# Performance work log

Hardware: AMD Instinct MI355X
Metric: run time of the kernel (lower is better)

Reference implementation:

```python
import jax, jax.numpy as jnp
import numpy as np

N_NODES = 50000
N_EDGES = 800000
IN_DIM, HIDDEN, Z_DIM = 32, 64, 32


def gcn_conv(x, W, b, src, dst, n):
    """PyG-style GCNConv: h = D^{-1/2}(A+I)D^{-1/2} (x W) + b."""
    h = x @ W  # [N, out]
    loop = jnp.arange(n, dtype=src.dtype)
    s = jnp.concatenate([src, loop])  # add self-loops
    d = jnp.concatenate([dst, loop])
    deg = jax.ops.segment_sum(jnp.ones(s.shape, h.dtype), d, num_segments=n)
    dinv = jax.lax.rsqrt(jnp.maximum(deg, jnp.asarray(1.0, h.dtype)))
    norm = dinv[s] * dinv[d]                       # [E+N]
    msg = h[s] * norm[:, None]                     # gather + scale
    out = jax.ops.segment_sum(msg, d, num_segments=n)  # scatter-add
    return out + b


def setup_inputs() -> dict:
    key = jax.random.key(0)
    ks = jax.random.split(key, 8)
    sc = lambda fan_in: 1.0 / np.sqrt(fan_in)
    x = jax.random.normal(ks[0], (N_NODES, IN_DIM), jnp.float32)
    edge_index = jax.random.randint(ks[1], (2, N_EDGES), 0, N_NODES, jnp.int64)
    W1 = jax.random.normal(ks[2], (IN_DIM, HIDDEN), jnp.float32) * sc(IN_DIM)
    b1 = jnp.zeros((HIDDEN,), jnp.float32)
    W2 = jax.random.normal(ks[3], (HIDDEN, HIDDEN), jnp.float32) * sc(HIDDEN)
    b2 = jnp.zeros((HIDDEN,), jnp.float32)
    W_mu = jax.random.normal(ks[4], (HIDDEN, Z_DIM), jnp.float32) * sc(HIDDEN)
    b_mu = jnp.zeros((Z_DIM,), jnp.float32)
    W_lv = jax.random.normal(ks[5], (HIDDEN, Z_DIM), jnp.float32) * sc(HIDDEN)
    b_lv = jnp.zeros((Z_DIM,), jnp.float32)
    eps = jax.random.normal(ks[6], (N_NODES, Z_DIM), jnp.float32)
    return {"x": x, "edge_index": edge_index, "W1": W1, "b1": b1, "W2": W2,
            "b2": b2, "W_mu": W_mu, "b_mu": b_mu, "W_lv": W_lv, "b_lv": b_lv,
            "eps": eps}


def reference(x, edge_index, W1, b1, W2, b2, W_mu, b_mu, W_lv, b_lv, eps):
    src, dst = edge_index[0], edge_index[1]
    n = x.shape[0]
    h = jax.nn.relu(gcn_conv(x, W1, b1, src, dst, n))
    h = jax.nn.relu(gcn_conv(h, W2, b2, src, dst, n))
    # dropout p=0.0 -> identity
    mu = gcn_conv(h, W_mu, b_mu, src, dst, n)
    logvar = gcn_conv(h, W_lv, b_lv, src, dst, n)
    z = mu + jnp.exp(0.5 * logvar) * eps  # reparametrize
    return (z, mu, logvar)
```

## Files before the change

### kernel.cpp

```cpp
#include <hip/hip_runtime.h>
#include <math.h>

#define N_NODES 50000
#define N_EDGES 800000
#define IN_DIM 32
#define HIDDEN 64
#define Z_DIM 32
#define SCAN_B 256
#define NB_SCAN ((N_NODES + SCAN_B - 1) / SCAN_B)
#define N_XCD 8
#define NPX ((N_NODES + N_XCD - 1) / N_XCD)
#define SLICE 2048
#define N_SLICE ((N_EDGES + SLICE - 1) / SLICE)
#define SCAT_B (N_SLICE * N_XCD)
#define FB 1024
#define CPAD 16

__device__ __forceinline__ unsigned short f2bf(float f) {
    unsigned int u = __float_as_uint(f);
    u += 0x7fffu + ((u >> 16) & 1u);
    return (unsigned short)(u >> 16);
}

__device__ __forceinline__ int detect64(const int* raw) {
    int lane = threadIdx.x & 63;
    int odd = raw[2 * lane + 1];
    unsigned long long b = __ballot(odd != 0);
    return (b == 0ULL) ? 1 : 0;
}

__device__ __forceinline__ void fma8(float w, uint4 f, float acc[8]) {
    acc[0] = fmaf(w, __uint_as_float(f.x << 16),         acc[0]);
    acc[1] = fmaf(w, __uint_as_float(f.x & 0xffff0000u), acc[1]);
    acc[2] = fmaf(w, __uint_as_float(f.y << 16),         acc[2]);
    acc[3] = fmaf(w, __uint_as_float(f.y & 0xffff0000u), acc[3]);
    acc[4] = fmaf(w, __uint_as_float(f.z << 16),         acc[4]);
    acc[5] = fmaf(w, __uint_as_float(f.z & 0xffff0000u), acc[5]);
    acc[6] = fmaf(w, __uint_as_float(f.w << 16),         acc[6]);
    acc[7] = fmaf(w, __uint_as_float(f.w & 0xffff0000u), acc[7]);
}
__device__ __forceinline__ void mul8(float w, uint4 f, float acc[8]) {
    acc[0] = w * __uint_as_float(f.x << 16);
    acc[1] = w * __uint_as_float(f.x & 0xffff0000u);
    acc[2] = w * __uint_as_float(f.y << 16);
    acc[3] = w * __uint_as_float(f.y & 0xffff0000u);
    acc[4] = w * __uint_as_float(f.z << 16);
    acc[5] = w * __uint_as_float(f.z & 0xffff0000u);
    acc[6] = w * __uint_as_float(f.w << 16);
    acc[7] = w * __uint_as_float(f.w & 0xffff0000u);
}

__global__ void prep_a_kernel(const float* __restrict__ x, unsigned short* __restrict__ xb,
                              const void* __restrict__ raw, ushort2* __restrict__ ep0,
                              int* __restrict__ cnt) {
    int is64 = detect64((const int*)raw);
    int i = blockIdx.x * 256 + threadIdx.x;
    if (i < N_NODES * IN_DIM) xb[i] = f2bf(x[i]);
    if (i < N_NODES * CPAD) cnt[i] = 0;
    if (i < N_EDGES) {
        int s, d;
        if (is64) {
            s = (int)((const long long*)raw)[i];
            d = (int)((const long long*)raw)[N_EDGES + i];
        } else {
            s = ((const int*)raw)[i];
            d = ((const int*)raw)[N_EDGES + i];
        }
        ep0[i] = make_ushort2((unsigned short)s, (unsigned short)d);
    }
}

__global__ __launch_bounds__(256) void hist_kernel(const ushort2* __restrict__ ep0,
                                                   int* __restrict__ cnt,
                                                   unsigned short* __restrict__ rank) {
    int xcd = blockIdx.x % N_XCD;
    int sl  = blockIdx.x / N_XCD;
    int lo  = xcd * NPX, hi = lo + NPX;
    int base = sl * SLICE;
#pragma unroll
    for (int j = 0; j < SLICE / 256; j++) {
        int e = base + j * 256 + threadIdx.x;
        if (e < N_EDGES) {
            int d = ep0[e].y;
            if (d >= lo && d < hi)
                rank[e] = (unsigned short)atomicAdd(&cnt[(size_t)d * CPAD], 1);
        }
    }
}

__global__ void scan1_kernel(const int* __restrict__ cnt, int* __restrict__ pre,
                             int* __restrict__ bsum, float* __restrict__ dinv) {
    __shared__ int s[SCAN_B];
    int t = threadIdx.x;
    int g = blockIdx.x * SCAN_B + t;
    int v = (g < N_NODES) ? cnt[(size_t)g * CPAD] : 0;
    if (g < N_NODES) dinv[g] = rsqrtf((float)(v + 1));
    s[t] = v;
    __syncthreads();
    for (int o = 1; o < SCAN_B; o <<= 1) {
        int add = (t >= o) ? s[t - o] : 0;
        __syncthreads();
        s[t] += add;
        __syncthreads();
    }
    if (g < N_NODES) pre[g] = s[t] - v;
    if (t == SCAN_B - 1) bsum[blockIdx.x] = s[t];
}

#define BSUM_SCAN_PROLOGUE(bsum, sb, sx)                                    \
    {                                                                       \
        int t_ = threadIdx.x;                                               \
        int bv_ = (t_ < NB_SCAN) ? bsum[t_] : 0;                            \
        sb[t_] = bv_;                                                       \
        __syncthreads();                                                    \
        for (int o_ = 1; o_ < 256; o_ <<= 1) {                              \
            int a_ = (t_ >= o_) ? sb[t_ - o_] : 0;                          \
            __syncthreads();                                                \
            sb[t_] += a_;                                                   \
            __syncthreads();                                                \
        }                                                                   \
        sx[t_] = sb[t_] - bv_;                                              \
        __syncthreads();                                                    \
    }

__global__ __launch_bounds__(256) void scatter_kernel(
        const ushort2* __restrict__ ep0, const unsigned short* __restrict__ rank,
        const int* __restrict__ pre, const int* __restrict__ bsum,
        const float* __restrict__ dinv, int2* __restrict__ ep) {
    __shared__ int sb[256];
    __shared__ int sx[256];
    BSUM_SCAN_PROLOGUE(bsum, sb, sx)
    int base = blockIdx.x * SLICE;
#pragma unroll
    for (int j = 0; j < SLICE / 256; j++) {
        int e = base + j * 256 + threadIdx.x;
        if (e < N_EDGES) {
            ushort2 sd = ep0[e];
            int d = sd.y;
            int p = pre[d] + sx[d >> 8] + (int)rank[e];
            int s = sd.x;
            ep[p] = make_int2(s, __float_as_int(dinv[s]));
        }
    }
}

__device__ __forceinline__ void agg64(int e0, int e1, int2 pr,
                                      const int2* __restrict__ ep,
                                      const uint4* __restrict__ g4,
                                      int2* eb, int lane, int gsel, int c,
                                      float acc[8]) {
    for (int b0 = e0; b0 < e1; b0 += 64) {
        int cnt = e1 - b0; cnt = cnt > 64 ? 64 : cnt;
        eb[lane] = pr;
        for (int j = 0; j < cnt; j += 16) {
            int2 ew0 = eb[j + gsel];
            int2 ew1 = eb[j + 8 + gsel];
            uint4 f0 = g4[(size_t)ew0.x * 8 + c];
            uint4 f1 = g4[(size_t)ew1.x * 8 + c];
            fma8(__int_as_float(ew0.y), f0, acc);
            fma8(__int_as_float(ew1.y), f1, acc);
        }
        if (b0 + 64 < e1) {
            pr = make_int2(0, 0);
            int idx = b0 + 64 + lane;
            if (idx < e1) pr = ep[idx];
        }
    }
}

__device__ __forceinline__ void agg32(int e0, int e1, int2 pr,
                                      const int2* __restrict__ ep,
                                      const uint4* __restrict__ x4,
                                      int2* eb, int lane, int gsel, int c,
                                      float acc[8]) {
    for (int b0 = e0; b0 < e1; b0 += 64) {
        int cnt = e1 - b0; cnt = cnt > 64 ? 64 : cnt;
        eb[lane] = pr;
        for (int j = 0; j < cnt; j += 32) {
            int2 ew0 = eb[j + gsel];
            int2 ew1 = eb[j + 16 + gsel];
            uint4 f0 = x4[(size_t)ew0.x * 4 + c];
            uint4 f1 = x4[(size_t)ew1.x * 4 + c];
            fma8(__int_as_float(ew0.y), f0, acc);
            fma8(__int_as_float(ew1.y), f1, acc);
        }
        if (b0 + 64 < e1) {
            pr = make_int2(0, 0);
            int idx = b0 + 64 + lane;
            if (idx < e1) pr = ep[idx];
        }
    }
}

__global__ __launch_bounds__(256) void fused_layer32_kernel(
        const int* __restrict__ pre, const int* __restrict__ bsum,
        const int2* __restrict__ ep, const float* __restrict__ dinv,
        const unsigned short* __restrict__ xb,
        const float* __restrict__ W1, const float* __restrict__ b1,
        unsigned short* __restrict__ out) {
    __shared__ int sb[256];
    __shared__ int sx[256];
    __shared__ int2 ebuf[4][64];
    __shared__ float sq[4][32];
    BSUM_SCAN_PROLOGUE(bsum, sb, sx)
    int lane = threadIdx.x & 63;
    int wav  = threadIdx.x >> 6;
    int gsel = lane >> 2;
    int c    = lane & 3;
    const uint4* x4 = (const uint4*)xb;
    int2* eb = &ebuf[wav][0];
    float wcol[IN_DIM];
#pragma unroll
    for (int k = 0; k < IN_DIM; k++) wcol[k] = W1[k * 64 + lane];
    float bb = b1[lane];
    int wid = __builtin_amdgcn_readfirstlane((int)((blockIdx.x * blockDim.x + threadIdx.x) >> 6));
    int nw  = (gridDim.x * blockDim.x) >> 6;
    int v = wid;
    if (v >= N_NODES) return;
    int e0 = pre[v] + sx[v >> 8];
    int e1 = (v + 1 < N_NODES) ? pre[v + 1] + sx[(v + 1) >> 8] : N_EDGES;
    float dv = dinv[v];
    uint4 hv = x4[(size_t)v * 4 + c];
    int2 pr = make_int2(0, 0);
    if (lane < e1 - e0) pr = ep[e0 + lane];
    while (v < N_NODES) {
        int vn = v + nw;
        int e0n = 0, e1n = 0;
        float dvn = 0.0f;
        uint4 hvn = make_uint4(0, 0, 0, 0);
        int2 prn = make_int2(0, 0);
        if (vn < N_NODES) {
            e0n = pre[vn] + sx[vn >> 8];
            e1n = (vn + 1 < N_NODES) ? pre[vn + 1] + sx[(vn + 1) >> 8] : N_EDGES;
            dvn = dinv[vn];
            hvn = x4[(size_t)vn * 4 + c];
            if (lane < e1n - e0n) prn = ep[e0n + lane];
        }
        float sv = (gsel == 0) ? dv : 0.0f;
        float acc[8];
        mul8(sv, hv, acc);
        agg32(e0, e1, pr, ep, x4, eb, lane, gsel, c, acc);
#pragma unroll
        for (int i = 0; i < 8; i++) {
            acc[i] += __shfl_xor(acc[i], 4);
            acc[i] += __shfl_xor(acc[i], 8);
            acc[i] += __shfl_xor(acc[i], 16);
            acc[i] += __shfl_xor(acc[i], 32);
        }
        if (lane < 4) {
            float4* qd = (float4*)(&sq[wav][lane * 8]);
            qd[0] = make_float4(dv * acc[0], dv * acc[1], dv * acc[2], dv * acc[3]);
            qd[1] = make_float4(dv * acc[4], dv * acc[5], dv * acc[6], dv * acc[7]);
        }
        float o0 = bb, o1 = 0.0f, o2 = 0.0f, o3 = 0.0f;
        const float4* q4 = (const float4*)(&sq[wav][0]);
#pragma unroll
        for (int k = 0; k < IN_DIM / 4; k++) {
            float4 tq = q4[k];
            o0 = fmaf(tq.x, wcol[4 * k + 0], o0);
            o1 = fmaf(tq.y, wcol[4 * k + 1], o1);
            o2 = fmaf(tq.z, wcol[4 * k + 2], o2);
            o3 = fmaf(tq.w, wcol[4 * k + 3], o3);
        }
        float o = (o0 + o1) + (o2 + o3);
        out[(size_t)v * 64 + lane] = f2bf(fmaxf(o, 0.0f));
        v = vn; e0 = e0n; e1 = e1n; dv = dvn; hv = hvn; pr = prn;
    }
}

__global__ __launch_bounds__(256) void fused_layer64_kernel(
        const int* __restrict__ pre, const int* __restrict__ bsum,
        const int2* __restrict__ ep, const float* __restrict__ dinv,
        const unsigned short* __restrict__ g,
        const float* __restrict__ W, const float* __restrict__ bias,
        unsigned short* __restrict__ out) {
    __shared__ int sb[256];
    __shared__ int sx[256];
    __shared__ int2 ebuf[4][64];
    __shared__ float sq[4][64];
    BSUM_SCAN_PROLOGUE(bsum, sb, sx)
    int lane = threadIdx.x & 63;
    int wav  = threadIdx.x >> 6;
    int gsel = lane >> 3;
    int c    = lane & 7;
    const uint4* g4 = (const uint4*)g;
    int2* eb = &ebuf[wav][0];
    float wcol[HIDDEN];
#pragma unroll
    for (int k = 0; k < HIDDEN; k++) wcol[k] = W[k * 64 + lane];
    float bb = bias[lane];
    int wid = __builtin_amdgcn_readfirstlane((int)((blockIdx.x * blockDim.x + threadIdx.x) >> 6));
    int nw  = (gridDim.x * blockDim.x) >> 6;
    int v = wid;
    if (v >= N_NODES) return;
    int e0 = pre[v] + sx[v >> 8];
    int e1 = (v + 1 < N_NODES) ? pre[v + 1] + sx[(v + 1) >> 8] : N_EDGES;
    float dv = dinv[v];
    uint4 hv = g4[(size_t)v * 8 + c];
    int2 pr = make_int2(0, 0);
    if (lane < e1 - e0) pr = ep[e0 + lane];
    while (v < N_NODES) {
        int vn = v + nw;
        int e0n = 0, e1n = 0;
        float dvn = 0.0f;
        uint4 hvn = make_uint4(0, 0, 0, 0);
        int2 prn = make_int2(0, 0);
        if (vn < N_NODES) {
            e0n = pre[vn] + sx[vn >> 8];
            e1n = (vn + 1 < N_NODES) ? pre[vn + 1] + sx[(vn + 1) >> 8] : N_EDGES;
            dvn = dinv[vn];
            hvn = g4[(size_t)vn * 8 + c];
            if (lane < e1n - e0n) prn = ep[e0n + lane];
        }
        float sv = (gsel == 0) ? dv : 0.0f;
        float acc[8];
        mul8(sv, hv, acc);
        agg64(e0, e1, pr, ep, g4, eb, lane, gsel, c, acc);
#pragma unroll
        for (int i = 0; i < 8; i++) {
            acc[i] += __shfl_xor(acc[i], 8);
            acc[i] += __shfl_xor(acc[i], 16);
            acc[i] += __shfl_xor(acc[i], 32);
        }
        if (lane < 8) {
            float4* qd = (float4*)(&sq[wav][lane * 8]);
            qd[0] = make_float4(dv * acc[0], dv * acc[1], dv * acc[2], dv * acc[3]);
            qd[1] = make_float4(dv * acc[4], dv * acc[5], dv * acc[6], dv * acc[7]);
        }
        float o0 = bb, o1 = 0.0f, o2 = 0.0f, o3 = 0.0f;
        const float4* q4 = (const float4*)(&sq[wav][0]);
#pragma unroll
        for (int k = 0; k < HIDDEN / 4; k++) {
            float4 tq = q4[k];
            o0 = fmaf(tq.x, wcol[4 * k + 0], o0);
            o1 = fmaf(tq.y, wcol[4 * k + 1], o1);
            o2 = fmaf(tq.z, wcol[4 * k + 2], o2);
            o3 = fmaf(tq.w, wcol[4 * k + 3], o3);
        }
        float o = (o0 + o1) + (o2 + o3);
        out[(size_t)v * 64 + lane] = f2bf(fmaxf(o, 0.0f));
        v = vn; e0 = e0n; e1 = e1n; dv = dvn; hv = hvn; pr = prn;
    }
}

__global__ __launch_bounds__(256) void fused_head_kernel(
        const int* __restrict__ pre, const int* __restrict__ bsum,
        const int2* __restrict__ ep, const float* __restrict__ dinv,
        const unsigned short* __restrict__ g,
        const float* __restrict__ Wmu, const float* __restrict__ Wlv,
        const float* __restrict__ bmu, const float* __restrict__ blv,
        const float* __restrict__ eps, float* __restrict__ outz) {
    __shared__ int sb[256];
    __shared__ int sx[256];
    __shared__ int2 ebuf[4][64];
    __shared__ float sq[4][64];
    BSUM_SCAN_PROLOGUE(bsum, sb, sx)
    int lane = threadIdx.x & 63;
    int wav  = threadIdx.x >> 6;
    int gsel = lane >> 3;
    int c    = lane & 7;
    int f = lane & 31;
    bool hi = lane >= 32;
    const uint4* g4 = (const uint4*)g;
    int2* eb = &ebuf[wav][0];
    float wcol[HIDDEN];
#pragma unroll
    for (int k = 0; k < HIDDEN; k++)
        wcol[k] = hi ? Wlv[k * 32 + f] : Wmu[k * 32 + f];
    float bb = hi ? blv[f] : bmu[f];
    float* z  = outz;
    float* mu = outz + (size_t)N_NODES * Z_DIM;
    float* lv = outz + 2 * (size_t)N_NODES * Z_DIM;
    int wid = __builtin_amdgcn_readfirstlane((int)((blockIdx.x * blockDim.x + threadIdx.x) >> 6));
    int nw  = (gridDim.x * blockDim.x) >> 6;
    int v = wid;
    if (v >= N_NODES) return;
    int e0 = pre[v] + sx[v >> 8];
    int e1 = (v + 1 < N_NODES) ? pre[v + 1] + sx[(v + 1) >> 8] : N_EDGES;
    float dv = dinv[v];
    uint4 hv = g4[(size_t)v * 8 + c];
    int2 pr = make_int2(0, 0);
    if (lane < e1 - e0) pr = ep[e0 + lane];
    while (v < N_NODES) {
        int vn = v + nw;
        int e0n = 0, e1n = 0;
        float dvn = 0.0f;
        uint4 hvn = make_uint4(0, 0, 0, 0);
        int2 prn = make_int2(0, 0);
        if (vn < N_NODES) {
            e0n = pre[vn] + sx[vn >> 8];
            e1n = (vn + 1 < N_NODES) ? pre[vn + 1] + sx[(vn + 1) >> 8] : N_EDGES;
            dvn = dinv[vn];
            hvn = g4[(size_t)vn * 8 + c];
            if (lane < e1n - e0n) prn = ep[e0n + lane];
        }
        float sv = (gsel == 0) ? dv : 0.0f;
        float acc[8];
        mul8(sv, hv, acc);
        agg64(e0, e1, pr, ep, g4, eb, lane, gsel, c, acc);
#pragma unroll
        for (int i = 0; i < 8; i++) {
            acc[i] += __shfl_xor(acc[i], 8);
            acc[i] += __shfl_xor(acc[i], 16);
            acc[i] += __shfl_xor(acc[i], 32);
        }
        if (lane < 8) {
            float4* qd = (float4*)(&sq[wav][lane * 8]);
            qd[0] = make_float4(dv * acc[0], dv * acc[1], dv * acc[2], dv * acc[3]);
            qd[1] = make_float4(dv * acc[4], dv * acc[5], dv * acc[6], dv * acc[7]);
        }
        float m0 = bb, m1 = 0.0f, m2 = 0.0f, m3 = 0.0f;
        const float4* q4 = (const float4*)(&sq[wav][0]);
#pragma unroll
        for (int k = 0; k < HIDDEN / 4; k++) {
            float4 tq = q4[k];
            m0 = fmaf(tq.x, wcol[4 * k + 0], m0);
            m1 = fmaf(tq.y, wcol[4 * k + 1], m1);
            m2 = fmaf(tq.z, wcol[4 * k + 2], m2);
            m3 = fmaf(tq.w, wcol[4 * k + 3], m3);
        }
        float m = (m0 + m1) + (m2 + m3);
        float ev = eps[(size_t)v * Z_DIM + f];
        float t  = expf(0.5f * m) * ev;
        float tlo = __shfl(t, lane | 32);
        size_t o = (size_t)v * Z_DIM + f;
        if (!hi) { mu[o] = m; z[o] = m + tlo; }
        else     { lv[o] = m; }
        v = vn; e0 = e0n; e1 = e1n; dv = dvn; hv = hvn; pr = prn;
    }
}

extern "C" void kernel_launch(void* const* d_in, const int* in_sizes, int n_in,
                              void* d_out, int out_size, void* d_ws, size_t ws_size,
                              hipStream_t stream) {
    const float* x   = (const float*)d_in[0];
    const void*  ei  = d_in[1];
    const float* W1  = (const float*)d_in[2];
    const float* b1  = (const float*)d_in[3];
    const float* W2  = (const float*)d_in[4];
    const float* b2  = (const float*)d_in[5];
    const float* Wmu = (const float*)d_in[6];
    const float* bmu = (const float*)d_in[7];
    const float* Wlv = (const float*)d_in[8];
    const float* blv = (const float*)d_in[9];
    const float* eps = (const float*)d_in[10];
    float* out = (float*)d_out;
    (void)in_sizes; (void)n_in; (void)out_size; (void)ws_size;

    char* ws = (char*)d_ws;
    size_t off = 0;
    auto alloc = [&](size_t bytes) -> void* {
        void* p = ws + off;
        off += (bytes + 255) & ~(size_t)255;
        return p;
    };
    int2*           ep     = (int2*)alloc(sizeof(int2) * N_EDGES);
    ushort2*        ep0    = (ushort2*)alloc(sizeof(ushort2) * N_EDGES);
    unsigned short* rank   = (unsigned short*)alloc(sizeof(short) * N_EDGES);
    int*            pre    = (int*)alloc(sizeof(int) * (N_NODES + 1));
    int*            cnt    = (int*)alloc(sizeof(int) * (size_t)N_NODES * CPAD);
    float*          dinv   = (float*)alloc(sizeof(float) * N_NODES);
    int*            bsum   = (int*)alloc(sizeof(int) * 256);
    unsigned short* xb     = (unsigned short*)alloc(sizeof(short) * (size_t)N_NODES * IN_DIM);
    unsigned short* G      = (unsigned short*)alloc(sizeof(short) * (size_t)N_NODES * HIDDEN);
    unsigned short* H      = (unsigned short*)alloc(sizeof(short) * (size_t)N_NODES * HIDDEN);

    prep_a_kernel<<<(N_NODES * IN_DIM + 255) / 256, 256, 0, stream>>>(x, xb, ei, ep0, cnt);
    hist_kernel<<<SCAT_B, 256, 0, stream>>>(ep0, cnt, rank);
    scan1_kernel<<<NB_SCAN, SCAN_B, 0, stream>>>(cnt, pre, bsum, dinv);
    scatter_kernel<<<N_SLICE, 256, 0, stream>>>(ep0, rank, pre, bsum, dinv, ep);
    fused_layer32_kernel<<<FB, 256, 0, stream>>>(pre, bsum, ep, dinv, xb, W1, b1, H);
    fused_layer64_kernel<<<FB, 256, 0, stream>>>(pre, bsum, ep, dinv, H, W2, b2, G);
    fused_head_kernel<<<FB, 256, 0, stream>>>(pre, bsum, ep, dinv, G, Wmu, Wlv, bmu, blv, eps, out);
}
```

Before: 249.1 us.

## Stage layer weights in LDS and batch dense transform over four nodes

In all three fused GCN kernels, each lane's column of the weight matrix moves out of registers and into shared memory loaded once per block. Aggregated node features are buffered per wave for four consecutive nodes, and the small dense matvec plus output writes are then done for all four at once. This is meant to cut register pressure from the 32–64 per-lane weight registers, raising occupancy for the latency-bound gather loop, and to reuse each LDS weight read across four nodes. FB is also doubled. The trade-off is extra LDS traffic and footprint per block, which could itself limit occupancy.

```diff
diff --git a/kernel.cpp b/kernel.cpp
--- a/kernel.cpp
+++ b/kernel.cpp
@@ -13,7 +13,7 @@
 #define SLICE 2048
 #define N_SLICE ((N_EDGES + SLICE - 1) / SLICE)
 #define SCAT_B (N_SLICE * N_XCD)
-#define FB 1024
+#define FB 2048
 #define CPAD 16
 
 __device__ __forceinline__ unsigned short f2bf(float f) {
@@ -201,7 +201,9 @@
     __shared__ int sb[256];
     __shared__ int sx[256];
     __shared__ int2 ebuf[4][64];
-    __shared__ float sq[4][32];
+    __shared__ float sq[4][4][IN_DIM];
+    __shared__ float wlds[IN_DIM * 64];
+    for (int i = threadIdx.x; i < IN_DIM * 64; i += 256) wlds[i] = W1[i];
     BSUM_SCAN_PROLOGUE(bsum, sb, sx)
     int lane = threadIdx.x & 63;
     int wav  = threadIdx.x >> 6;
@@ -209,9 +211,6 @@
     int c    = lane & 3;
     const uint4* x4 = (const uint4*)xb;
     int2* eb = &ebuf[wav][0];
-    float wcol[IN_DIM];
-#pragma unroll
-    for (int k = 0; k < IN_DIM; k++) wcol[k] = W1[k * 64 + lane];
     float bb = b1[lane];
     int wid = __builtin_amdgcn_readfirstlane((int)((blockIdx.x * blockDim.x + threadIdx.x) >> 6));
     int nw  = (gridDim.x * blockDim.x) >> 6;
@@ -223,6 +222,7 @@
     uint4 hv = x4[(size_t)v * 4 + c];
     int2 pr = make_int2(0, 0);
     if (lane < e1 - e0) pr = ep[e0 + lane];
+    int nb = 0, vbase = v;
     while (v < N_NODES) {
         int vn = v + nw;
         int e0n = 0, e1n = 0;
@@ -248,22 +248,38 @@
             acc[i] += __shfl_xor(acc[i], 32);
         }
         if (lane < 4) {
-            float4* qd = (float4*)(&sq[wav][lane * 8]);
+            float4* qd = (float4*)(&sq[wav][nb][lane * 8]);
             qd[0] = make_float4(dv * acc[0], dv * acc[1], dv * acc[2], dv * acc[3]);
             qd[1] = make_float4(dv * acc[4], dv * acc[5], dv * acc[6], dv * acc[7]);
         }
-        float o0 = bb, o1 = 0.0f, o2 = 0.0f, o3 = 0.0f;
-        const float4* q4 = (const float4*)(&sq[wav][0]);
-#pragma unroll
-        for (int k = 0; k < IN_DIM / 4; k++) {
-            float4 tq = q4[k];
-            o0 = fmaf(tq.x, wcol[4 * k + 0], o0);
-            o1 = fmaf(tq.y, wcol[4 * k + 1], o1);
-            o2 = fmaf(tq.z, wcol[4 * k + 2], o2);
-            o3 = fmaf(tq.w, wcol[4 * k + 3], o3);
-        }
-        float o = (o0 + o1) + (o2 + o3);
-        out[(size_t)v * 64 + lane] = f2bf(fmaxf(o, 0.0f));
+        nb++;
+        if (nb == 4 || vn >= N_NODES) {
+            float o0 = bb, o1 = bb, o2 = bb, o3 = bb;
+#pragma unroll
+            for (int k4 = 0; k4 < IN_DIM / 4; k4++) {
+                float4 q0 = *(const float4*)(&sq[wav][0][k4 * 4]);
+                float4 q1 = *(const float4*)(&sq[wav][1][k4 * 4]);
+                float4 q2 = *(const float4*)(&sq[wav][2][k4 * 4]);
+                float4 q3 = *(const float4*)(&sq[wav][3][k4 * 4]);
+                float w0 = wlds[(k4 * 4 + 0) * 64 + lane];
+                float w1 = wlds[(k4 * 4 + 1) * 64 + lane];
+                float w2 = wlds[(k4 * 4 + 2) * 64 + lane];
+                float w3 = wlds[(k4 * 4 + 3) * 64 + lane];
+                o0 = fmaf(q0.x, w0, o0); o0 = fmaf(q0.y, w1, o0);
+                o0 = fmaf(q0.z, w2, o0); o0 = fmaf(q0.w, w3, o0);
+                o1 = fmaf(q1.x, w0, o1); o1 = fmaf(q1.y, w1, o1);
+                o1 = fmaf(q1.z, w2, o1); o1 = fmaf(q1.w, w3, o1);
+                o2 = fmaf(q2.x, w0, o2); o2 = fmaf(q2.y, w1, o2);
+                o2 = fmaf(q2.z, w2, o2); o2 = fmaf(q2.w, w3, o2);
+                o3 = fmaf(q3.x, w0, o3); o3 = fmaf(q3.y, w1, o3);
+                o3 = fmaf(q3.z, w2, o3); o3 = fmaf(q3.w, w3, o3);
+            }
+            out[(size_t)vbase * 64 + lane] = f2bf(fmaxf(o0, 0.0f));
+            if (nb > 1) out[(size_t)(vbase + nw) * 64 + lane] = f2bf(fmaxf(o1, 0.0f));
+            if (nb > 2) out[(size_t)(vbase + 2 * nw) * 64 + lane] = f2bf(fmaxf(o2, 0.0f));
+            if (nb > 3) out[(size_t)(vbase + 3 * nw) * 64 + lane] = f2bf(fmaxf(o3, 0.0f));
+            nb = 0; vbase = vn;
+        }
         v = vn; e0 = e0n; e1 = e1n; dv = dvn; hv = hvn; pr = prn;
     }
 }
@@ -277,7 +293,9 @@
     __shared__ int sb[256];
     __shared__ int sx[256];
     __shared__ int2 ebuf[4][64];
-    __shared__ float sq[4][64];
+    __shared__ float sq[4][4][HIDDEN];
+    __shared__ float wlds[HIDDEN * 64];
+    for (int i = threadIdx.x; i < HIDDEN * 64; i += 256) wlds[i] = W[i];
     BSUM_SCAN_PROLOGUE(bsum, sb, sx)
     int lane = threadIdx.x & 63;
     int wav  = threadIdx.x >> 6;
@@ -285,9 +303,6 @@
     int c    = lane & 7;
     const uint4* g4 = (const uint4*)g;
     int2* eb = &ebuf[wav][0];
-    float wcol[HIDDEN];
-#pragma unroll
-    for (int k = 0; k < HIDDEN; k++) wcol[k] = W[k * 64 + lane];
     float bb = bias[lane];
     int wid = __builtin_amdgcn_readfirstlane((int)((blockIdx.x * blockDim.x + threadIdx.x) >> 6));
     int nw  = (gridDim.x * blockDim.x) >> 6;
@@ -299,6 +314,7 @@
     uint4 hv = g4[(size_t)v * 8 + c];
     int2 pr = make_int2(0, 0);
     if (lane < e1 - e0) pr = ep[e0 + lane];
+    int nb = 0, vbase = v;
     while (v < N_NODES) {
         int vn = v + nw;
         int e0n = 0, e1n = 0;
@@ -323,22 +339,38 @@
             acc[i] += __shfl_xor(acc[i], 32);
         }
         if (lane < 8) {
-            float4* qd = (float4*)(&sq[wav][lane * 8]);
+            float4* qd = (float4*)(&sq[wav][nb][lane * 8]);
             qd[0] = make_float4(dv * acc[0], dv * acc[1], dv * acc[2], dv * acc[3]);
             qd[1] = make_float4(dv * acc[4], dv * acc[5], dv * acc[6], dv * acc[7]);
         }
-        float o0 = bb, o1 = 0.0f, o2 = 0.0f, o3 = 0.0f;
-        const float4* q4 = (const float4*)(&sq[wav][0]);
-#pragma unroll
-        for (int k = 0; k < HIDDEN / 4; k++) {
-            float4 tq = q4[k];
-            o0 = fmaf(tq.x, wcol[4 * k + 0], o0);
-            o1 = fmaf(tq.y, wcol[4 * k + 1], o1);
-            o2 = fmaf(tq.z, wcol[4 * k + 2], o2);
-            o3 = fmaf(tq.w, wcol[4 * k + 3], o3);
-        }
-        float o = (o0 + o1) + (o2 + o3);
-        out[(size_t)v * 64 + lane] = f2bf(fmaxf(o, 0.0f));
+        nb++;
+        if (nb == 4 || vn >= N_NODES) {
+            float o0 = bb, o1 = bb, o2 = bb, o3 = bb;
+#pragma unroll
+            for (int k4 = 0; k4 < HIDDEN / 4; k4++) {
+                float4 q0 = *(const float4*)(&sq[wav][0][k4 * 4]);
+                float4 q1 = *(const float4*)(&sq[wav][1][k4 * 4]);
+                float4 q2 = *(const float4*)(&sq[wav][2][k4 * 4]);
+                float4 q3 = *(const float4*)(&sq[wav][3][k4 * 4]);
+                float w0 = wlds[(k4 * 4 + 0) * 64 + lane];
+                float w1 = wlds[(k4 * 4 + 1) * 64 + lane];
+                float w2 = wlds[(k4 * 4 + 2) * 64 + lane];
+                float w3 = wlds[(k4 * 4 + 3) * 64 + lane];
+                o0 = fmaf(q0.x, w0, o0); o0 = fmaf(q0.y, w1, o0);
+                o0 = fmaf(q0.z, w2, o0); o0 = fmaf(q0.w, w3, o0);
+                o1 = fmaf(q1.x, w0, o1); o1 = fmaf(q1.y, w1, o1);
+                o1 = fmaf(q1.z, w2, o1); o1 = fmaf(q1.w, w3, o1);
+                o2 = fmaf(q2.x, w0, o2); o2 = fmaf(q2.y, w1, o2);
+                o2 = fmaf(q2.z, w2, o2); o2 = fmaf(q2.w, w3, o2);
+                o3 = fmaf(q3.x, w0, o3); o3 = fmaf(q3.y, w1, o3);
+                o3 = fmaf(q3.z, w2, o3); o3 = fmaf(q3.w, w3, o3);
+            }
+            out[(size_t)vbase * 64 + lane] = f2bf(fmaxf(o0, 0.0f));
+            if (nb > 1) out[(size_t)(vbase + nw) * 64 + lane] = f2bf(fmaxf(o1, 0.0f));
+            if (nb > 2) out[(size_t)(vbase + 2 * nw) * 64 + lane] = f2bf(fmaxf(o2, 0.0f));
+            if (nb > 3) out[(size_t)(vbase + 3 * nw) * 64 + lane] = f2bf(fmaxf(o3, 0.0f));
+            nb = 0; vbase = vn;
+        }
         v = vn; e0 = e0n; e1 = e1n; dv = dvn; hv = hvn; pr = prn;
     }
 }
@@ -353,7 +385,12 @@
     __shared__ int sb[256];
     __shared__ int sx[256];
     __shared__ int2 ebuf[4][64];
-    __shared__ float sq[4][64];
+    __shared__ float sq[4][4][HIDDEN];
+    __shared__ float wlds[HIDDEN * 64];
+    for (int i = threadIdx.x; i < HIDDEN * 64; i += 256) {
+        int k = i >> 6, col = i & 63;
+        wlds[i] = (col < 32) ? Wmu[k * 32 + col] : Wlv[k * 32 + (col - 32)];
+    }
     BSUM_SCAN_PROLOGUE(bsum, sb, sx)
     int lane = threadIdx.x & 63;
     int wav  = threadIdx.x >> 6;
@@ -363,10 +400,6 @@
     bool hi = lane >= 32;
     const uint4* g4 = (const uint4*)g;
     int2* eb = &ebuf[wav][0];
-    float wcol[HIDDEN];
-#pragma unroll
-    for (int k = 0; k < HIDDEN; k++)
-        wcol[k] = hi ? Wlv[k * 32 + f] : Wmu[k * 32 + f];
     float bb = hi ? blv[f] : bmu[f];
     float* z  = outz;
     float* mu = outz + (size_t)N_NODES * Z_DIM;
@@ -381,6 +414,7 @@
     uint4 hv = g4[(size_t)v * 8 + c];
     int2 pr = make_int2(0, 0);
     if (lane < e1 - e0) pr = ep[e0 + lane];
+    int nb = 0, vbase = v;
     while (v < N_NODES) {
         int vn = v + nw;
         int e0n = 0, e1n = 0;
@@ -405,27 +439,47 @@
             acc[i] += __shfl_xor(acc[i], 32);
         }
         if (lane < 8) {
-            float4* qd = (float4*)(&sq[wav][lane * 8]);
+            float4* qd = (float4*)(&sq[wav][nb][lane * 8]);
             qd[0] = make_float4(dv * acc[0], dv * acc[1], dv * acc[2], dv * acc[3]);
             qd[1] = make_float4(dv * acc[4], dv * acc[5], dv * acc[6], dv * acc[7]);
         }
-        float m0 = bb, m1 = 0.0f, m2 = 0.0f, m3 = 0.0f;
-        const float4* q4 = (const float4*)(&sq[wav][0]);
-#pragma unroll
-        for (int k = 0; k < HIDDEN / 4; k++) {
-            float4 tq = q4[k];
-            m0 = fmaf(tq.x, wcol[4 * k + 0], m0);
-            m1 = fmaf(tq.y, wcol[4 * k + 1], m1);
-            m2 = fmaf(tq.z, wcol[4 * k + 2], m2);
-            m3 = fmaf(tq.w, wcol[4 * k + 3], m3);
-        }
-        float m = (m0 + m1) + (m2 + m3);
-        float ev = eps[(size_t)v * Z_DIM + f];
-        float t  = expf(0.5f * m) * ev;
-        float tlo = __shfl(t, lane | 32);
-        size_t o = (size_t)v * Z_DIM + f;
-        if (!hi) { mu[o] = m; z[o] = m + tlo; }
-        else     { lv[o] = m; }
+        nb++;
+        if (nb == 4 || vn >= N_NODES) {
+            float o0 = bb, o1 = bb, o2 = bb, o3 = bb;
+#pragma unroll
+            for (int k4 = 0; k4 < HIDDEN / 4; k4++) {
+                float4 q0 = *(const float4*)(&sq[wav][0][k4 * 4]);
+                float4 q1 = *(const float4*)(&sq[wav][1][k4 * 4]);
+                float4 q2 = *(const float4*)(&sq[wav][2][k4 * 4]);
+                float4 q3 = *(const float4*)(&sq[wav][3][k4 * 4]);
+                float w0 = wlds[(k4 * 4 + 0) * 64 + lane];
+                float w1 = wlds[(k4 * 4 + 1) * 64 + lane];
+                float w2 = wlds[(k4 * 4 + 2) * 64 + lane];
+                float w3 = wlds[(k4 * 4 + 3) * 64 + lane];
+                o0 = fmaf(q0.x, w0, o0); o0 = fmaf(q0.y, w1, o0);
+                o0 = fmaf(q0.z, w2, o0); o0 = fmaf(q0.w, w3, o0);
+                o1 = fmaf(q1.x, w0, o1); o1 = fmaf(q1.y, w1, o1);
+                o1 = fmaf(q1.z, w2, o1); o1 = fmaf(q1.w, w3, o1);
+                o2 = fmaf(q2.x, w0, o2); o2 = fmaf(q2.y, w1, o2);
+                o2 = fmaf(q2.z, w2, o2); o2 = fmaf(q2.w, w3, o2);
+                o3 = fmaf(q3.x, w0, o3); o3 = fmaf(q3.y, w1, o3);
+                o3 = fmaf(q3.z, w2, o3); o3 = fmaf(q3.w, w3, o3);
+            }
+#pragma unroll
+            for (int n = 0; n < 4; n++) {
+                if (n < nb) {
+                    int vv = vbase + n * nw;
+                    float m = (n == 0) ? o0 : (n == 1) ? o1 : (n == 2) ? o2 : o3;
+                    float ev = eps[(size_t)vv * Z_DIM + f];
+                    float t  = expf(0.5f * m) * ev;
+                    float tlo = __shfl(t, lane | 32);
+                    size_t o = (size_t)vv * Z_DIM + f;
+                    if (!hi) { mu[o] = m; z[o] = m + tlo; }
+                    else     { lv[o] = m; }
+                }
+            }
+            nb = 0; vbase = vn;
+        }
         v = vn; e0 = e0n; e1 = e1n; dv = dvn; hv = hvn; pr = prn;
     }
 }
```

Result: slower. 425.0 us (+70.6%).
